# Performance work log

Hardware: AMD Instinct MI355X
Metric: run time of the kernel (lower is better)

## Reference

```python
import jax, jax.numpy as jnp
import numpy as np

B, C_IN, C_OUT, N, K = 4, 128, 128, 4096, 32
BN_EPS = 1e-5


def setup_inputs() -> dict:
    key = jax.random.key(0)
    ks = jax.random.split(key, 12)
    x = jax.random.normal(ks[0], (B, C_IN, N), jnp.float32)
    feature = jax.random.normal(ks[1], (B, C_OUT, N, K), jnp.float32)
    graph_index = jax.random.randint(ks[2], (B, N, K), 0, N)
    s_in = 1.0 / np.sqrt(C_IN)
    s_out = 1.0 / np.sqrt(C_OUT)
    # theta_x: Conv2d(C_IN -> C_IN, 1x1), shared for theta and phi branches
    Wt = jax.random.uniform(ks[3], (C_IN, C_IN), jnp.float32, -s_in, s_in)
    bt = jax.random.uniform(ks[4], (C_IN,), jnp.float32, -s_in, s_in)
    # g: Conv2d(C_OUT -> C_OUT, 1x1)
    Wg = jax.random.uniform(ks[5], (C_OUT, C_OUT), jnp.float32, -s_out, s_out)
    bg = jax.random.uniform(ks[6], (C_OUT,), jnp.float32, -s_out, s_out)
    # W: Conv1d(C_OUT -> C_OUT, 1) followed by BatchNorm1d(C_OUT)
    Ww = jax.random.uniform(ks[7], (C_OUT, C_OUT), jnp.float32, -s_out, s_out)
    bw = jax.random.uniform(ks[8], (C_OUT,), jnp.float32, -s_out, s_out)
    gamma = jnp.ones((C_OUT,), jnp.float32)
    beta = jnp.zeros((C_OUT,), jnp.float32)
    return {"graph_index": graph_index, "x": x, "feature": feature,
            "Wt": Wt, "bt": bt, "Wg": Wg, "bg": bg,
            "Ww": Ww, "bw": bw, "gamma": gamma, "beta": beta}


def reference(graph_index, x, feature, Wt, bt, Wg, bg, Ww, bw, gamma, beta):
    b, c, n = x.shape
    # torch does x.contiguous().view(B, N, C) -> a reshape, not a transpose
    xr = x.reshape(b, n, c)                                   # [B,N,C]
    # index_points: per-batch gather of k neighbors
    batch_idx = jnp.arange(b)[:, None, None]
    nb = xr[batch_idx, graph_index]                           # [B,N,K,C]
    # theta_x 1x1 conv applied to centre and to neighbors (shared weights)
    theta = jnp.einsum('bnc,dc->bnd', xr, Wt) + bt            # [B,N,C]
    phi = jnp.einsum('bnkc,dc->bnkd', nb, Wt) + bt            # [B,N,K,C]
    # local attention logits over k neighbors, softmax over k
    logits = jnp.einsum('bnd,bnkd->bnk', theta, phi)          # [B,N,K]
    coef = jax.nn.softmax(logits, axis=-1)                    # [B,N,K]
    # g 1x1 conv on neighbor value features
    gx = jnp.einsum('bcnk,dc->bnkd', feature, Wg) + bg        # [B,N,K,Cout]
    # weighted aggregation over neighbors
    out = jnp.einsum('bnk,bnkd->bnd', coef, gx)               # [B,N,Cout]
    # W: 1x1 Conv1d then BatchNorm1d (training-mode batch stats)
    y = jnp.einsum('bnd,ed->ben', out, Ww) + bw[None, :, None]  # [B,Cout,N]
    mean = jnp.mean(y, axis=(0, 2), keepdims=True)
    var = jnp.var(y, axis=(0, 2), keepdims=True)
    z = (y - mean) * jax.lax.rsqrt(var + BN_EPS)
    z = z * gamma[None, :, None] + beta[None, :, None]
    return z
```

## Files before the change

### kernel.cpp

```cpp
#include <hip/hip_runtime.h>
#include <hip/hip_bf16.h>

#define BB 4
#define CC 128
#define NN 4096
#define KK 32
#define THETA_OFF  0
#define THETA_SZ   (BB*NN*CC)
#define M_OFF      (THETA_OFF + THETA_SZ)
#define M_SZ       (CC*CC)
#define B2_OFF     (M_OFF + M_SZ)
#define COEF_OFF   (B2_OFF + 128)
#define COEF_SZ    (BB*NN*KK)
#define PART_OFF   (COEF_OFF + COEF_SZ)
#define PART_SZ    (1024*256)
#define PART2_OFF  (PART_OFF + PART_SZ)
#define PART2_SZ   (64*256)

__device__ __forceinline__ float dot4(float4 a, float4 b) {
    return a.x*b.x + a.y*b.y + a.z*b.z + a.w*b.w;
}

__device__ __forceinline__ void async_copy16(const float* g, float* l) {
    __builtin_amdgcn_global_load_lds(
        (const __attribute__((address_space(1))) void*)g,
        (__attribute__((address_space(3))) void*)l, 16, 0, 0);
}

__device__ __forceinline__ int wswz(int e, int q) {
    return (q ^ (e & 7) ^ ((e >> 3) & 3)) * 4;
}

__global__ __launch_bounds__(256) void kWT(const float* __restrict__ x,
                                           const float* __restrict__ Wt,
                                           const float* __restrict__ bt,
                                           float* __restrict__ theta) {
    __shared__ float xr[32][132];
    __shared__ float wt[128][32];
    int t = threadIdx.x;
    long base = (long)blockIdx.x * (32 * 128);
#pragma unroll
    for (int r = 0; r < 4; ++r) {
        int f = (t + 256*r) * 4;
        int dn = f >> 7, c = f & 127;
        *(float4*)&xr[dn][c] = *(const float4*)(x + base + f);
    }
    float acc[4][4] = {};
    int e0 = t & 31, dn0 = (t >> 5) * 4;
    for (int cb = 0; cb < 4; ++cb) {
        __syncthreads();
#pragma unroll
        for (int r = 0; r < 4; ++r) {
            int f = (t + 256*r) * 4;
            int d = f >> 5, cc = f & 31;
            *(float4*)&wt[d][wswz(d, cc >> 2)] = *(const float4*)(Wt + d*128 + cb*32 + cc);
        }
        __syncthreads();
#pragma unroll
        for (int q = 0; q < 8; ++q) {
            int sw = wswz(e0, q);
            float4 a4[4], m4[4];
#pragma unroll
            for (int j = 0; j < 4; ++j) a4[j] = *(const float4*)&xr[dn0+j][cb*32 + q*4];
#pragma unroll
            for (int i = 0; i < 4; ++i) m4[i] = *(const float4*)&wt[e0 + 32*i][sw];
#pragma unroll
            for (int i = 0; i < 4; ++i)
#pragma unroll
                for (int j = 0; j < 4; ++j)
                    acc[i][j] += dot4(a4[j], m4[i]);
        }
    }
    __syncthreads();
#pragma unroll
    for (int i = 0; i < 4; ++i) {
        float b = bt[e0 + 32*i];
#pragma unroll
        for (int j = 0; j < 4; ++j)
            xr[dn0 + j][e0 + 32*i] = acc[i][j] + b;
    }
    __syncthreads();
#pragma unroll
    for (int r = 0; r < 4; ++r) {
        int f = (t + 256*r) * 4;
        int dn = f >> 7, c = f & 127;
        *(float4*)(theta + base + f) = *(const float4*)&xr[dn][c];
    }
}

__global__ __launch_bounds__(256) void kA(const int* __restrict__ gi,
                                          const float* __restrict__ theta,
                                          const float* __restrict__ Ww,
                                          const float* __restrict__ Wg,
                                          const float* __restrict__ bg,
                                          const float* __restrict__ bw,
                                          float* __restrict__ M,
                                          float* __restrict__ b2,
                                          float* __restrict__ coefG) {
    int t = threadIdx.x;
    if (blockIdx.x >= 2048) {
        int bid2 = blockIdx.x - 2048;
        if (bid2 < 64) {
            int e = bid2 * 2 + (t >> 7);
            int c = t & 127;
            float acc = 0.f;
#pragma unroll 8
            for (int d = 0; d < 128; ++d)
                acc += Ww[e*128 + d] * Wg[d*128 + c];
            M[e*128 + c] = acc;
        } else if (t < 128) {
            float acc = bw[t];
            for (int d = 0; d < 128; ++d)
                acc += Ww[t*128 + d] * bg[d];
            b2[t] = acc;
        }
        return;
    }
    __shared__ float tc[8][132];
    __shared__ float logits[8][33];
    int bid = (blockIdx.x & 7) * 256 + (blockIdx.x >> 3);
    long trow0 = (long)bid * 8;
    int b = bid >> 9;
    int k = t >> 3, l8 = t & 7;
    {
        int f = t * 4;
        int dn = f >> 7, c = f & 127;
        *(float4*)&tc[dn][c] = *(const float4*)(theta + trow0*128 + f);
    }
    int idxs[8];
#pragma unroll
    for (int dn = 0; dn < 8; ++dn)
        idxs[dn] = gi[(trow0 + dn) * KK + k];
    __syncthreads();
    const float* tbat = theta + (long)b * NN * CC;
#pragma unroll 2
    for (int dn = 0; dn < 8; ++dn) {
        const float* row = tbat + (long)idxs[dn] * CC;
        float p = 0.f;
#pragma unroll
        for (int j = 0; j < 4; ++j) {
            int c = j*32 + l8*4;
            float4 g = *(const float4*)(row + c);
            float4 tcv = *(const float4*)&tc[dn][c];
            p += dot4(g, tcv);
        }
        p += __shfl_xor(p, 1);
        p += __shfl_xor(p, 2);
        p += __shfl_xor(p, 4);
        if (l8 == 0) logits[dn][k] = p;
    }
    __syncthreads();
    if (t < 64) {
        int row = t >> 3;
        float l[4];
#pragma unroll
        for (int j = 0; j < 4; ++j) l[j] = logits[row][l8 + 8*j];
        float m = fmaxf(fmaxf(l[0], l[1]), fmaxf(l[2], l[3]));
        m = fmaxf(m, __shfl_xor(m, 1));
        m = fmaxf(m, __shfl_xor(m, 2));
        m = fmaxf(m, __shfl_xor(m, 4));
        float e[4]; float s = 0.f;
#pragma unroll
        for (int j = 0; j < 4; ++j) { e[j] = __expf(l[j] - m); s += e[j]; }
        s += __shfl_xor(s, 1);
        s += __shfl_xor(s, 2);
        s += __shfl_xor(s, 4);
        float inv = 1.0f / s;
#pragma unroll
        for (int j = 0; j < 4; ++j)
            coefG[(trow0 + row) * KK + l8 + 8*j] = e[j] * inv;
    }
}

__global__ __launch_bounds__(256) void kBC(const float* __restrict__ coefG,
                                           const float* __restrict__ feat,
                                           const float* __restrict__ Mmat,
                                           const float* __restrict__ b2v,
                                           float* __restrict__ y,
                                           float* __restrict__ partial) {
    __shared__ float ring[4][2][512];
    __shared__ float aggL[16][132];
    int t = threadIdx.x;
    int bid = (blockIdx.x & 7) * 128 + (blockIdx.x >> 3);
    int b = bid >> 8;
    int n0 = (bid & 255) * 16;
    long trow0 = (long)bid * 16;
    int w = t >> 6, lane = t & 63;
    int r8 = lane >> 3, ks = lane & 7;

    float4 cf0 = *(const float4*)(coefG + (trow0 + r8) * KK + ks * 4);
    float4 cf1 = *(const float4*)(coefG + (trow0 + 8 + r8) * KK + ks * 4);
    asm volatile("" :: "v"(cf0.x), "v"(cf0.y), "v"(cf0.z), "v"(cf0.w));
    asm volatile("" :: "v"(cf1.x), "v"(cf1.y), "v"(cf1.z), "v"(cf1.w));

    const size_t S = (size_t)NN * KK;
    const float* fbase = feat + (size_t)b * CC * S + (size_t)n0 * KK + lane * 4;
    float* myRing = &ring[w][0][0];

#pragma unroll
    for (int ch = 0; ch < 2; ++ch) {
        const float* fc = fbase + (size_t)(ch * 4 + w) * S;
        float* ld = myRing + ch * 512;
        async_copy16(fc, ld);
        async_copy16(fc + 256, ld + 256);
    }

#pragma unroll
    for (int ch = 0; ch < 32; ++ch) {
        if (ch < 31) asm volatile("s_waitcnt vmcnt(2)" ::: "memory");
        else         asm volatile("s_waitcnt vmcnt(0)" ::: "memory");
        const float* sl = myRing + (ch & 1) * 512 + lane * 4;
        float4 f0 = *(const float4*)(sl);
        float4 f1 = *(const float4*)(sl + 256);
        float v0 = dot4(f0, cf0);
        float v1 = dot4(f1, cf1);
        v0 += __shfl_xor(v0, 1); v0 += __shfl_xor(v0, 2); v0 += __shfl_xor(v0, 4);
        v1 += __shfl_xor(v1, 1); v1 += __shfl_xor(v1, 2); v1 += __shfl_xor(v1, 4);
        if (ks == 0) {
            aggL[r8][ch * 4 + w]     = v0;
            aggL[8 + r8][ch * 4 + w] = v1;
        }
        if (ch + 2 < 32) {
            const float* fc = fbase + (size_t)((ch + 2) * 4 + w) * S;
            float* ld = myRing + (ch & 1) * 512;
            async_copy16(fc, ld);
            async_copy16(fc + 256, ld + 256);
        }
    }
    __syncthreads();

    float (*mc)[32] = (float(*)[32])&ring[0][0][0];
    float acc[4][2] = {};
    int e0 = t & 31, dn0 = (t >> 5) * 2;
    for (int cb = 0; cb < 4; ++cb) {
        __syncthreads();
#pragma unroll
        for (int r = 0; r < 4; ++r) {
            int f = (t + 256*r) * 4;
            int e = f >> 5, cc = f & 31;
            *(float4*)&mc[e][wswz(e, cc >> 2)] = *(const float4*)(Mmat + e*128 + cb*32 + cc);
        }
        __syncthreads();
#pragma unroll
        for (int q = 0; q < 8; ++q) {
            int sw = wswz(e0, q);
            float4 a4[2], m4[4];
#pragma unroll
            for (int j = 0; j < 2; ++j) a4[j] = *(const float4*)&aggL[dn0+j][cb*32 + q*4];
#pragma unroll
            for (int i = 0; i < 4; ++i) m4[i] = *(const float4*)&mc[e0 + 32*i][sw];
#pragma unroll
            for (int i = 0; i < 4; ++i)
#pragma unroll
                for (int j = 0; j < 2; ++j)
                    acc[i][j] += dot4(a4[j], m4[i]);
        }
    }
    __syncthreads();
    float (*yT)[20] = (float(*)[20])&ring[0][0][0];
#pragma unroll
    for (int i = 0; i < 4; ++i) {
        int e = e0 + 32*i;
        float bb = b2v[e];
#pragma unroll
        for (int j = 0; j < 2; ++j)
            yT[e][dn0 + j] = acc[i][j] + bb;
    }
    __syncthreads();
    {
        int e = t >> 1, half = t & 1;
        float4 v0 = *(const float4*)&yT[e][half * 8];
        float4 v1 = *(const float4*)&yT[e][half * 8 + 4];
        float* dst = y + ((size_t)(b*CC + e)) * NN + n0 + half * 8;
        *(float4*)dst       = v0;
        *(float4*)(dst + 4) = v1;
    }
    if (t < 128) {
        float s = 0.f, q = 0.f;
#pragma unroll
        for (int j = 0; j < 16; ++j) {
            float v = yT[t][j];
            s += v; q += v * v;
        }
        partial[(size_t)bid * 256 + t]       = s;
        partial[(size_t)bid * 256 + 128 + t] = q;
    }
}

__global__ __launch_bounds__(256) void kR1(const float* __restrict__ partial,
                                           float* __restrict__ partial2) {
    int t = threadIdx.x;
    long b0 = (long)blockIdx.x * 16;
    float acc = 0.f;
#pragma unroll
    for (int j = 0; j < 16; ++j)
        acc += partial[(b0 + j) * 256 + t];
    partial2[(long)blockIdx.x * 256 + t] = acc;
}

__global__ __launch_bounds__(256) void kZf(float* __restrict__ y,
                                           const float* __restrict__ partial2,
                                           const float* __restrict__ gamma,
                                           const float* __restrict__ beta) {
    __shared__ float buf[256];
    __shared__ float scs[128];
    __shared__ float shs[128];
    int t = threadIdx.x;
    float acc = 0.f;
#pragma unroll 8
    for (int j = 0; j < 64; ++j)
        acc += partial2[j * 256 + t];
    buf[t] = acc;
    __syncthreads();
    if (t < 128) {
        float S = buf[t], Q = buf[t + 128];
        const float invN = 1.0f / (BB * NN);
        float mean = S * invN;
        float var  = Q * invN - mean * mean;
        float sc = rsqrtf(var + 1e-5f) * gamma[t];
        scs[t] = sc;
        shs[t] = beta[t] - mean * sc;
    }
    __syncthreads();
    int idx = blockIdx.x * 256 + t;
#pragma unroll
    for (int r = 0; r < 2; ++r) {
        int i = idx + r * 262144;
        int e = (i >> 10) & 127;
        float sc = scs[e], sh = shs[e];
        float4 v = ((float4*)y)[i];
        v.x = v.x * sc + sh;
        v.y = v.y * sc + sh;
        v.z = v.z * sc + sh;
        v.w = v.w * sc + sh;
        ((float4*)y)[i] = v;
    }
}

extern "C" void kernel_launch(void* const* d_in, const int* in_sizes, int n_in,
                              void* d_out, int out_size, void* d_ws, size_t ws_size,
                              hipStream_t stream) {
    const int*   gi    = (const int*)d_in[0];
    const float* x     = (const float*)d_in[1];
    const float* feat  = (const float*)d_in[2];
    const float* Wt    = (const float*)d_in[3];
    const float* bt    = (const float*)d_in[4];
    const float* Wg    = (const float*)d_in[5];
    const float* bg    = (const float*)d_in[6];
    const float* Ww    = (const float*)d_in[7];
    const float* bw    = (const float*)d_in[8];
    const float* gamma = (const float*)d_in[9];
    const float* beta  = (const float*)d_in[10];

    float* y  = (float*)d_out;
    float* ws = (float*)d_ws;
    float* theta    = ws + THETA_OFF;
    float* Mmat     = ws + M_OFF;
    float* b2       = ws + B2_OFF;
    float* coefG    = ws + COEF_OFF;
    float* partial  = ws + PART_OFF;
    float* partial2 = ws + PART2_OFF;

    kWT<<<512, 256, 0, stream>>>(x, Wt, bt, theta);
    kA<<<2113, 256, 0, stream>>>(gi, theta, Ww, Wg, bg, bw, Mmat, b2, coefG);
    kBC<<<1024, 256, 0, stream>>>(coefG, feat, Mmat, b2, y, partial);
    kR1<<<64, 256, 0, stream>>>(partial, partial2);
    kZf<<<1024, 256, 0, stream>>>(y, partial2, gamma, beta);
}
```

Baseline: 94.97 us.

## Fuse attention-logit softmax into aggregation kernel and move M precompute into theta kernel

The separate kA kernel is removed. The Ww*Wg and bias precompute blocks move into the theta-projection kernel as extra blocks. The neighbor-gather, logits and softmax now run at the start of kBC, per 16-row tile, with coefficients kept in LDS. This drops one launch and the global round trip of the coefficient array, and shared memory is reused through a union. The cost is that the gather latency now sits in front of the feature streaming inside kBC, and LDS use per block goes up.

```diff
diff --git a/kernel.cpp b/kernel.cpp
--- a/kernel.cpp
+++ b/kernel.cpp
@@ -10,9 +10,7 @@
 #define M_OFF      (THETA_OFF + THETA_SZ)
 #define M_SZ       (CC*CC)
 #define B2_OFF     (M_OFF + M_SZ)
-#define COEF_OFF   (B2_OFF + 128)
-#define COEF_SZ    (BB*NN*KK)
-#define PART_OFF   (COEF_OFF + COEF_SZ)
+#define PART_OFF   (B2_OFF + 128)
 #define PART_SZ    (1024*256)
 #define PART2_OFF  (PART_OFF + PART_SZ)
 #define PART2_SZ   (64*256)
@@ -34,72 +32,18 @@
 __global__ __launch_bounds__(256) void kWT(const float* __restrict__ x,
                                            const float* __restrict__ Wt,
                                            const float* __restrict__ bt,
-                                           float* __restrict__ theta) {
+                                           const float* __restrict__ Ww,
+                                           const float* __restrict__ Wg,
+                                           const float* __restrict__ bg,
+                                           const float* __restrict__ bw,
+                                           float* __restrict__ theta,
+                                           float* __restrict__ M,
+                                           float* __restrict__ b2) {
     __shared__ float xr[32][132];
     __shared__ float wt[128][32];
     int t = threadIdx.x;
-    long base = (long)blockIdx.x * (32 * 128);
-#pragma unroll
-    for (int r = 0; r < 4; ++r) {
-        int f = (t + 256*r) * 4;
-        int dn = f >> 7, c = f & 127;
-        *(float4*)&xr[dn][c] = *(const float4*)(x + base + f);
-    }
-    float acc[4][4] = {};
-    int e0 = t & 31, dn0 = (t >> 5) * 4;
-    for (int cb = 0; cb < 4; ++cb) {
-        __syncthreads();
-#pragma unroll
-        for (int r = 0; r < 4; ++r) {
-            int f = (t + 256*r) * 4;
-            int d = f >> 5, cc = f & 31;
-            *(float4*)&wt[d][wswz(d, cc >> 2)] = *(const float4*)(Wt + d*128 + cb*32 + cc);
-        }
-        __syncthreads();
-#pragma unroll
-        for (int q = 0; q < 8; ++q) {
-            int sw = wswz(e0, q);
-            float4 a4[4], m4[4];
-#pragma unroll
-            for (int j = 0; j < 4; ++j) a4[j] = *(const float4*)&xr[dn0+j][cb*32 + q*4];
-#pragma unroll
-            for (int i = 0; i < 4; ++i) m4[i] = *(const float4*)&wt[e0 + 32*i][sw];
-#pragma unroll
-            for (int i = 0; i < 4; ++i)
-#pragma unroll
-                for (int j = 0; j < 4; ++j)
-                    acc[i][j] += dot4(a4[j], m4[i]);
-        }
-    }
-    __syncthreads();
-#pragma unroll
-    for (int i = 0; i < 4; ++i) {
-        float b = bt[e0 + 32*i];
-#pragma unroll
-        for (int j = 0; j < 4; ++j)
-            xr[dn0 + j][e0 + 32*i] = acc[i][j] + b;
-    }
-    __syncthreads();
-#pragma unroll
-    for (int r = 0; r < 4; ++r) {
-        int f = (t + 256*r) * 4;
-        int dn = f >> 7, c = f & 127;
-        *(float4*)(theta + base + f) = *(const float4*)&xr[dn][c];
-    }
-}
-
-__global__ __launch_bounds__(256) void kA(const int* __restrict__ gi,
-                                          const float* __restrict__ theta,
-                                          const float* __restrict__ Ww,
-                                          const float* __restrict__ Wg,
-                                          const float* __restrict__ bg,
-                                          const float* __restrict__ bw,
-                                          float* __restrict__ M,
-                                          float* __restrict__ b2,
-                                          float* __restrict__ coefG) {
-    int t = threadIdx.x;
-    if (blockIdx.x >= 2048) {
-        int bid2 = blockIdx.x - 2048;
+    if (blockIdx.x >= 512) {
+        int bid2 = blockIdx.x - 512;
         if (bid2 < 64) {
             int e = bid2 * 2 + (t >> 7);
             int c = t & 127;
@@ -116,69 +60,72 @@
         }
         return;
     }
-    __shared__ float tc[8][132];
-    __shared__ float logits[8][33];
-    int bid = (blockIdx.x & 7) * 256 + (blockIdx.x >> 3);
-    long trow0 = (long)bid * 8;
-    int b = bid >> 9;
-    int k = t >> 3, l8 = t & 7;
-    {
-        int f = t * 4;
+    long base = (long)blockIdx.x * (32 * 128);
+#pragma unroll
+    for (int r = 0; r < 4; ++r) {
+        int f = (t + 256*r) * 4;
         int dn = f >> 7, c = f & 127;
-        *(float4*)&tc[dn][c] = *(const float4*)(theta + trow0*128 + f);
-    }
-    int idxs[8];
-#pragma unroll
-    for (int dn = 0; dn < 8; ++dn)
-        idxs[dn] = gi[(trow0 + dn) * KK + k];
-    __syncthreads();
-    const float* tbat = theta + (long)b * NN * CC;
-#pragma unroll 2
-    for (int dn = 0; dn < 8; ++dn) {
-        const float* row = tbat + (long)idxs[dn] * CC;
-        float p = 0.f;
-#pragma unroll
-        for (int j = 0; j < 4; ++j) {
-            int c = j*32 + l8*4;
-            float4 g = *(const float4*)(row + c);
-            float4 tcv = *(const float4*)&tc[dn][c];
-            p += dot4(g, tcv);
-        }
-        p += __shfl_xor(p, 1);
-        p += __shfl_xor(p, 2);
-        p += __shfl_xor(p, 4);
-        if (l8 == 0) logits[dn][k] = p;
-    }
-    __syncthreads();
-    if (t < 64) {
-        int row = t >> 3;
-        float l[4];
-#pragma unroll
-        for (int j = 0; j < 4; ++j) l[j] = logits[row][l8 + 8*j];
-        float m = fmaxf(fmaxf(l[0], l[1]), fmaxf(l[2], l[3]));
-        m = fmaxf(m, __shfl_xor(m, 1));
-        m = fmaxf(m, __shfl_xor(m, 2));
-        m = fmaxf(m, __shfl_xor(m, 4));
-        float e[4]; float s = 0.f;
-#pragma unroll
-        for (int j = 0; j < 4; ++j) { e[j] = __expf(l[j] - m); s += e[j]; }
-        s += __shfl_xor(s, 1);
-        s += __shfl_xor(s, 2);
-        s += __shfl_xor(s, 4);
-        float inv = 1.0f / s;
+        *(float4*)&xr[dn][c] = *(const float4*)(x + base + f);
+    }
+    float acc[4][4] = {};
+    int e0 = t & 31, dn0 = (t >> 5) * 4;
+    for (int cb = 0; cb < 4; ++cb) {
+        __syncthreads();
+#pragma unroll
+        for (int r = 0; r < 4; ++r) {
+            int f = (t + 256*r) * 4;
+            int d = f >> 5, cc = f & 31;
+            *(float4*)&wt[d][wswz(d, cc >> 2)] = *(const float4*)(Wt + d*128 + cb*32 + cc);
+        }
+        __syncthreads();
+#pragma unroll
+        for (int q = 0; q < 8; ++q) {
+            int sw = wswz(e0, q);
+            float4 a4[4], m4[4];
+#pragma unroll
+            for (int j = 0; j < 4; ++j) a4[j] = *(const float4*)&xr[dn0+j][cb*32 + q*4];
+#pragma unroll
+            for (int i = 0; i < 4; ++i) m4[i] = *(const float4*)&wt[e0 + 32*i][sw];
+#pragma unroll
+            for (int i = 0; i < 4; ++i)
+#pragma unroll
+                for (int j = 0; j < 4; ++j)
+                    acc[i][j] += dot4(a4[j], m4[i]);
+        }
+    }
+    __syncthreads();
+#pragma unroll
+    for (int i = 0; i < 4; ++i) {
+        float b = bt[e0 + 32*i];
 #pragma unroll
         for (int j = 0; j < 4; ++j)
-            coefG[(trow0 + row) * KK + l8 + 8*j] = e[j] * inv;
-    }
-}
-
-__global__ __launch_bounds__(256) void kBC(const float* __restrict__ coefG,
+            xr[dn0 + j][e0 + 32*i] = acc[i][j] + b;
+    }
+    __syncthreads();
+#pragma unroll
+    for (int r = 0; r < 4; ++r) {
+        int f = (t + 256*r) * 4;
+        int dn = f >> 7, c = f & 127;
+        *(float4*)(theta + base + f) = *(const float4*)&xr[dn][c];
+    }
+}
+
+union GU {
+    struct { float tc[16][132]; float logits[16][33]; } g;
+    float ring[4][2][512];
+    float mc[128][32];
+    float yT[128][20];
+};
+
+__global__ __launch_bounds__(256) void kBC(const int* __restrict__ gi,
+                                           const float* __restrict__ theta,
                                            const float* __restrict__ feat,
                                            const float* __restrict__ Mmat,
                                            const float* __restrict__ b2v,
                                            float* __restrict__ y,
                                            float* __restrict__ partial) {
-    __shared__ float ring[4][2][512];
+    __shared__ GU u;
+    __shared__ float coefL[16][36];
     __shared__ float aggL[16][132];
     int t = threadIdx.x;
     int bid = (blockIdx.x & 7) * 128 + (blockIdx.x >> 3);
@@ -188,14 +135,65 @@
     int w = t >> 6, lane = t & 63;
     int r8 = lane >> 3, ks = lane & 7;
 
-    float4 cf0 = *(const float4*)(coefG + (trow0 + r8) * KK + ks * 4);
-    float4 cf1 = *(const float4*)(coefG + (trow0 + 8 + r8) * KK + ks * 4);
-    asm volatile("" :: "v"(cf0.x), "v"(cf0.y), "v"(cf0.z), "v"(cf0.w));
-    asm volatile("" :: "v"(cf1.x), "v"(cf1.y), "v"(cf1.z), "v"(cf1.w));
+    {
+        int k = t >> 3, l8 = t & 7;
+#pragma unroll
+        for (int r = 0; r < 2; ++r) {
+            int f = (t + 256*r) * 4;
+            int dn = f >> 7, c = f & 127;
+            *(float4*)&u.g.tc[dn][c] = *(const float4*)(theta + trow0*128 + f);
+        }
+        int idxs[16];
+#pragma unroll
+        for (int dn = 0; dn < 16; ++dn)
+            idxs[dn] = gi[(trow0 + dn) * KK + k];
+        __syncthreads();
+        const float* tbat = theta + (long)b * NN * CC;
+#pragma unroll 2
+        for (int dn = 0; dn < 16; ++dn) {
+            const float* row = tbat + (long)idxs[dn] * CC;
+            float p = 0.f;
+#pragma unroll
+            for (int j = 0; j < 4; ++j) {
+                int c = j*32 + l8*4;
+                float4 g = *(const float4*)(row + c);
+                float4 tcv = *(const float4*)&u.g.tc[dn][c];
+                p += dot4(g, tcv);
+            }
+            p += __shfl_xor(p, 1);
+            p += __shfl_xor(p, 2);
+            p += __shfl_xor(p, 4);
+            if (l8 == 0) u.g.logits[dn][k] = p;
+        }
+        __syncthreads();
+        if (t < 128) {
+            int row = t >> 3;
+            float l[4];
+#pragma unroll
+            for (int j = 0; j < 4; ++j) l[j] = u.g.logits[row][l8 + 8*j];
+            float m = fmaxf(fmaxf(l[0], l[1]), fmaxf(l[2], l[3]));
+            m = fmaxf(m, __shfl_xor(m, 1));
+            m = fmaxf(m, __shfl_xor(m, 2));
+            m = fmaxf(m, __shfl_xor(m, 4));
+            float e[4]; float s = 0.f;
+#pragma unroll
+            for (int j = 0; j < 4; ++j) { e[j] = __expf(l[j] - m); s += e[j]; }
+            s += __shfl_xor(s, 1);
+            s += __shfl_xor(s, 2);
+            s += __shfl_xor(s, 4);
+            float inv = 1.0f / s;
+#pragma unroll
+            for (int j = 0; j < 4; ++j) coefL[row][l8 + 8*j] = e[j] * inv;
+        }
+        __syncthreads();
+    }
+
+    float4 cf0 = *(const float4*)&coefL[r8][ks * 4];
+    float4 cf1 = *(const float4*)&coefL[8 + r8][ks * 4];
 
     const size_t S = (size_t)NN * KK;
     const float* fbase = feat + (size_t)b * CC * S + (size_t)n0 * KK + lane * 4;
-    float* myRing = &ring[w][0][0];
+    float* myRing = &u.ring[w][0][0];
 
 #pragma unroll
     for (int ch = 0; ch < 2; ++ch) {
@@ -229,7 +227,6 @@
     }
     __syncthreads();
 
-    float (*mc)[32] = (float(*)[32])&ring[0][0][0];
     float acc[4][2] = {};
     int e0 = t & 31, dn0 = (t >> 5) * 2;
     for (int cb = 0; cb < 4; ++cb) {
@@ -238,7 +235,7 @@
         for (int r = 0; r < 4; ++r) {
             int f = (t + 256*r) * 4;
             int e = f >> 5, cc = f & 31;
-            *(float4*)&mc[e][wswz(e, cc >> 2)] = *(const float4*)(Mmat + e*128 + cb*32 + cc);
+            *(float4*)&u.mc[e][wswz(e, cc >> 2)] = *(const float4*)(Mmat + e*128 + cb*32 + cc);
         }
         __syncthreads();
 #pragma unroll
@@ -248,7 +245,7 @@
 #pragma unroll
             for (int j = 0; j < 2; ++j) a4[j] = *(const float4*)&aggL[dn0+j][cb*32 + q*4];
 #pragma unroll
-            for (int i = 0; i < 4; ++i) m4[i] = *(const float4*)&mc[e0 + 32*i][sw];
+            for (int i = 0; i < 4; ++i) m4[i] = *(const float4*)&u.mc[e0 + 32*i][sw];
 #pragma unroll
             for (int i = 0; i < 4; ++i)
 #pragma unroll
@@ -257,20 +254,19 @@
         }
     }
     __syncthreads();
-    float (*yT)[20] = (float(*)[20])&ring[0][0][0];
 #pragma unroll
     for (int i = 0; i < 4; ++i) {
         int e = e0 + 32*i;
         float bb = b2v[e];
 #pragma unroll
         for (int j = 0; j < 2; ++j)
-            yT[e][dn0 + j] = acc[i][j] + bb;
+            u.yT[e][dn0 + j] = acc[i][j] + bb;
     }
     __syncthreads();
     {
         int e = t >> 1, half = t & 1;
-        float4 v0 = *(const float4*)&yT[e][half * 8];
-        float4 v1 = *(const float4*)&yT[e][half * 8 + 4];
+        float4 v0 = *(const float4*)&u.yT[e][half * 8];
+        float4 v1 = *(const float4*)&u.yT[e][half * 8 + 4];
         float* dst = y + ((size_t)(b*CC + e)) * NN + n0 + half * 8;
         *(float4*)dst       = v0;
         *(float4*)(dst + 4) = v1;
@@ -279,7 +275,7 @@
         float s = 0.f, q = 0.f;
 #pragma unroll
         for (int j = 0; j < 16; ++j) {
-            float v = yT[t][j];
+            float v = u.yT[t][j];
             s += v; q += v * v;
         }
         partial[(size_t)bid * 256 + t]       = s;
@@ -357,13 +353,11 @@
     float* theta    = ws + THETA_OFF;
     float* Mmat     = ws + M_OFF;
     float* b2       = ws + B2_OFF;
-    float* coefG    = ws + COEF_OFF;
     float* partial  = ws + PART_OFF;
     float* partial2 = ws + PART2_OFF;
 
-    kWT<<<512, 256, 0, stream>>>(x, Wt, bt, theta);
-    kA<<<2113, 256, 0, stream>>>(gi, theta, Ww, Wg, bg, bw, Mmat, b2, coefG);
-    kBC<<<1024, 256, 0, stream>>>(coefG, feat, Mmat, b2, y, partial);
+    kWT<<<577, 256, 0, stream>>>(x, Wt, bt, Ww, Wg, bg, bw, theta, Mmat, b2);
+    kBC<<<1024, 256, 0, stream>>>(gi, theta, feat, Mmat, b2, y, partial);
     kR1<<<64, 256, 0, stream>>>(partial, partial2);
     kZf<<<1024, 256, 0, stream>>>(y, partial2, gamma, beta);
 }
```

Measured after the change: 112.6 us. +18.5%, slower.
